# Optimization experiments

Measured on AMD Instinct MI355X. Metric: run time of the kernel, lower is better.

The kernel has to match this reference:

```python
import jax, jax.numpy as jnp
import numpy as np
from jax import lax

U = 512      # rnn_units
A = 512      # attn_units
E = 300      # embed_dim
VS = 30000   # source vocab
VT = 30000   # target vocab
S = 64       # source len
T = 32       # target len
B = 32       # batch


def gru_step(h, x, Wih, Whh, bih, bhh):
    # PyTorch GRU cell: r,z,n gate order
    gi = x @ Wih.T + bih
    gh = h @ Whh.T + bhh
    ir, iz, i_n = jnp.split(gi, 3, axis=-1)
    hr, hz, h_n = jnp.split(gh, 3, axis=-1)
    r = jax.nn.sigmoid(ir + hr)
    z = jax.nn.sigmoid(iz + hz)
    n = jnp.tanh(i_n + r * h_n)
    return (1.0 - z) * n + z * h


def setup_inputs() -> dict:
    key = jax.random.key(0)
    ks = jax.random.split(key, 24)
    w = lambda k, shape, s=0.08: jax.random.normal(k, shape, dtype=jnp.float32) * s
    inp = {
        "emb_src": w(ks[0], (VS, E), 0.1),
        "emb_trg": w(ks[1], (VT, E), 0.1),
        # encoder bidirectional GRU (fwd/bwd directions)
        "enc_Wih_f": w(ks[2], (3 * U, E)), "enc_Whh_f": w(ks[3], (3 * U, U)),
        "enc_bih_f": w(ks[4], (3 * U,)), "enc_bhh_f": w(ks[5], (3 * U,)),
        "enc_Wih_b": w(ks[6], (3 * U, E)), "enc_Whh_b": w(ks[7], (3 * U, U)),
        "enc_bih_b": w(ks[8], (3 * U,)), "enc_bhh_b": w(ks[9], (3 * U,)),
        "enc_Wfc": w(ks[10], (U, 2 * U)), "enc_bfc": w(ks[11], (U,)),
        # attention fc: attn_in = 3U -> A
        "attn_W": w(ks[12], (A, 3 * U)), "attn_b": w(ks[13], (A,)),
        # decoder GRU: input = 2U + E
        "dec_Wih": w(ks[14], (3 * U, 2 * U + E)), "dec_Whh": w(ks[15], (3 * U, U)),
        "dec_bih": w(ks[16], (3 * U,)), "dec_bhh": w(ks[17], (3 * U,)),
        # decoder output fc: 3U + E -> VT
        "dec_Wfc": w(ks[18], (VT, 3 * U + E)), "dec_bfc": w(ks[19], (VT,)),
        "source": jax.random.randint(ks[20], (S, B), 0, VS, dtype=jnp.int32),
        "target": jax.random.randint(ks[21], (T, B), 0, VT, dtype=jnp.int32),
    }
    return inp


def reference(emb_src, emb_trg,
              enc_Wih_f, enc_Whh_f, enc_bih_f, enc_bhh_f,
              enc_Wih_b, enc_Whh_b, enc_bih_b, enc_bhh_b,
              enc_Wfc, enc_bfc, attn_W, attn_b,
              dec_Wih, dec_Whh, dec_bih, dec_bhh, dec_Wfc, dec_bfc,
              source, target):
    # dropout in eval mode (identity); teacher_forcing fixed to 1.0 (deterministic)
    batch = source.shape[1]
    emb = emb_src[source]  # [S, B, E]
    h0 = jnp.zeros((batch, U), dtype=emb.dtype)

    def fstep(h, x):
        h2 = gru_step(h, x, enc_Wih_f, enc_Whh_f, enc_bih_f, enc_bhh_f)
        return h2, h2

    def bstep(h, x):
        h2 = gru_step(h, x, enc_Wih_b, enc_Whh_b, enc_bih_b, enc_bhh_b)
        return h2, h2

    hf, outs_f = lax.scan(fstep, h0, emb)
    hb, outs_b = lax.scan(bstep, h0, emb[::-1])
    outs_b = outs_b[::-1]
    enc_outputs = jnp.concatenate([outs_f, outs_b], axis=-1)        # [S, B, 2U]
    state = jnp.tanh(jnp.concatenate([hf, hb], axis=-1) @ enc_Wfc.T + enc_bfc)  # [B, U]
    enc_bt = jnp.transpose(enc_outputs, (1, 0, 2))                  # [B, S, 2U]

    def dstep(st, tok):
        emb_t = emb_trg[tok]                                        # [B, E]
        dec_rep = jnp.broadcast_to(st[:, None, :], (batch, enc_bt.shape[1], U))
        comb = jnp.concatenate([dec_rep, enc_bt], axis=2)           # [B, S, 3U]
        scores = jnp.tanh(jnp.einsum('bsf,af->bsa', comb, attn_W) + attn_b).sum(-1)
        wts = jax.nn.softmax(scores, axis=1)                        # [B, S]
        ctx = jnp.einsum('bs,bsh->bh', wts, enc_bt)                 # [B, 2U]
        x = jnp.concatenate([emb_t, ctx], axis=1)                   # [B, E+2U]
        st2 = gru_step(st, x, dec_Wih, dec_Whh, dec_bih, dec_bhh)   # [B, U]
        logits = jnp.concatenate([st2, ctx, emb_t], axis=1) @ dec_Wfc.T + dec_bfc
        return st2, logits

    _, logits = lax.scan(dstep, state, target[:-1])                 # [T-1, B, VT]
    zero_row = jnp.zeros((1, batch, dec_Wfc.shape[0]), dtype=logits.dtype)
    return jnp.concatenate([zero_row, logits], axis=0)              # [T, B, VT]
```

## Files before the change

### kernel.cpp

```cpp
#include <hip/hip_runtime.h>

#define UU 512
#define EE 300
#define VTT 30000
#define SS 64
#define TT 32
#define BB 32

typedef unsigned short u16;
typedef short s8v __attribute__((ext_vector_type(8)));
typedef unsigned short us4 __attribute__((ext_vector_type(4)));
typedef float f4v __attribute__((ext_vector_type(4)));

__device__ __forceinline__ float bf2f(u16 v){
  union { unsigned u; float f; } x; x.u = ((unsigned)v) << 16; return x.f;
}
__device__ __forceinline__ u16 f2bf(float f){
  union { float f; unsigned u; } x; x.f = f;
  unsigned r = x.u + 0x7FFFu + ((x.u >> 16) & 1u);
  return (u16)(r >> 16);
}
__device__ __forceinline__ float sigm(float x){ return 1.f / (1.f + __expf(-x)); }
__device__ __forceinline__ float ftanh(float x){
  float t = __expf(-2.f * fabsf(x));
  float r = (1.f - t) / (1.f + t);
  return x < 0.f ? -r : r;
}
__device__ __forceinline__ int imin(int a, int b){ return a < b ? a : b; }

__device__ __forceinline__ void gll16(const u16* g, u16* l){
  __builtin_amdgcn_global_load_lds(
      (const __attribute__((address_space(1))) void*)g,
      (__attribute__((address_space(3))) void*)l, 16, 0, 0);
}

__global__ void k_init(float* __restrict__ hF, float* __restrict__ out,
                       u16* __restrict__ Xl, float* __restrict__ hbfF){
  int i = blockIdx.x * 256 + threadIdx.x;
  if(i < 4*BB*UU) hF[i] = 0.f;
  if(i < BB*VTT) out[i] = 0.f;
  if(i < 992*20){
    int r = i / 20, c = i - r*20;
    Xl[(size_t)r*1856 + 1836 + c] = 0;
  }
  if(i < 65536) hbfF[i] = 0.f;
}

__global__ void k_embsrc(const float* __restrict__ emb, const int* __restrict__ src,
                         u16* __restrict__ X){
  int i = blockIdx.x * 256 + threadIdx.x;
  if(i >= SS*BB*320) return;
  int tb = i / 320, k = i - tb*320;
  X[i] = (k < EE) ? f2bf(emb[(size_t)src[tb]*EE + k]) : (u16)0;
}

__global__ void k_embT(const float* __restrict__ emb, const int* __restrict__ tgt,
                       u16* __restrict__ X, u16* __restrict__ Xl){
  int i = blockIdx.x * 256 + threadIdx.x;
  if(i >= 992*320) return;
  int r = i / 320, k = i - r*320;
  u16 v = (k < EE) ? f2bf(emb[(size_t)tgt[r]*EE + k]) : (u16)0;
  X[i] = v;
  if(k < EE) Xl[(size_t)r*1856 + 1536 + k] = v;
}

__global__ void k_cvt(const float* __restrict__ src, int srs, int cofs, int take,
                      u16* __restrict__ dst, int cdst){
  int r = blockIdx.x;
  const float* s = src + (size_t)r*srs + cofs;
  u16* d = dst + (size_t)r*cdst;
  for(int c4 = threadIdx.x; c4 < (cdst >> 2); c4 += blockDim.x){
    us4 o;
    if(c4*4 < take){
      f4v v = *(const f4v*)(s + c4*4);
      o[0]=f2bf(v[0]); o[1]=f2bf(v[1]); o[2]=f2bf(v[2]); o[3]=f2bf(v[3]);
    } else o = (us4){0,0,0,0};
    *(us4*)(d + c4*4) = o;
  }
}

__global__ void k_wprep(const float* __restrict__ W, int ldw, int colofs,
                        int gstr, int ng, int ubstr, int NKF, int passes,
                        int total, u16* __restrict__ out){
  int flat = blockIdx.x * 256 + threadIdx.x;
  if(flat >= total) return;
  int l = flat & 63;
  int g = (flat >> 6) % ng;
  int kf = (flat / (64*ng)) % NKF;
  int ub = flat / (64*ng*NKF);
  int row = g*gstr + ub*ubstr + (l & 15);
  int col = colofs + kf*32 + ((l >> 4) << 3);
  const float* s = W + (size_t)row*ldw + col;
  f4v v0 = *(const f4v*)(s);
  f4v v1 = *(const f4v*)(s + 4);
  size_t base = ((((size_t)(ub*NKF + kf)*ng + g)*passes)*64 + l)*8;
  us4 h0, h1;
  h0[0]=f2bf(v0[0]); h0[1]=f2bf(v0[1]); h0[2]=f2bf(v0[2]); h0[3]=f2bf(v0[3]);
  h1[0]=f2bf(v1[0]); h1[1]=f2bf(v1[1]); h1[2]=f2bf(v1[2]); h1[3]=f2bf(v1[3]);
// ... 42 lines not shown
  for(int k0 = 0; k0 < K; k0 += 32){
    __syncthreads();
    gll16(Ag0 + k0, Al0); gll16(Ag1 + k0, Al1);
    gll16(Bg0 + k0, Bl0); gll16(Bg1 + k0, Bl1);
    __syncthreads();
    s8v af[4], bfv[4];
    #pragma unroll
    for(int mi = 0; mi < 4; mi++)
      af[mi] = *(const s8v*)(Asl + (wm*64 + mi*16 + lm)*32 + lq*8);
    #pragma unroll
    for(int nj = 0; nj < 4; nj++)
      bfv[nj] = *(const s8v*)(Bsl + (wn*64 + nj*16 + lm)*32 + lq*8);
    #pragma unroll
    for(int mi = 0; mi < 4; mi++)
      #pragma unroll
      for(int nj = 0; nj < 4; nj++)
        acc[mi][nj] = __builtin_amdgcn_mfma_f32_16x16x32_bf16(af[mi], bfv[nj], acc[mi][nj], 0, 0, 0);
  }
  #pragma unroll
  for(int nj = 0; nj < 4; nj++){
    int n = n0 + wn*64 + nj*16 + lm;
    if(n < N){
      float bv = bias[n];
      #pragma unroll
      for(int mi = 0; mi < 4; mi++){
        #pragma unroll
        for(int rg = 0; rg < 4; rg++){
          int m = m0 + wm*64 + mi*16 + lq*4 + rg;
          if(m < M) C[(size_t)(m + mofs)*ldc + n] = acc[mi][nj][rg] + bv;
        }
      }
    }
  }
}

__global__ __launch_bounds__(256) void k_gemm_bf(
    const u16* __restrict__ A, int lda, const u16* __restrict__ B, int ldb,
    const float* __restrict__ bias, float* __restrict__ C, int ldc, int mofs,
    int M, int N, int K){
  gemm_body(blockIdx.x*128, blockIdx.y*128, A, lda, B, ldb, bias, C, ldc, mofs, M, N, K);
}

__global__ __launch_bounds__(256) void k_gemm_lg(
    const u16* __restrict__ A, int lda, const u16* __restrict__ B, int ldb,
    const float* __restrict__ bias, float* __restrict__ C, int ldc, int mofs,
    int M, int N, int K){
  int id = blockIdx.x;
  int x = id & 7, j = id >> 3;
  int m = j & 7, p = (j & ~7) | x;
  if(p * 128 >= N) return;
  gemm_body(m*128, p*128, A, lda, B, ldb, bias, C, ldc, mofs, M, N, K);
}

__global__ __launch_bounds__(64) void k_encs(int t,
    const float* __restrict__ gi_f, const float* __restrict__ gi_b,
    const u16* __restrict__ Wenc,
    const float* __restrict__ bhh_f, const float* __restrict__ bhh_b,
    float* __restrict__ hF, u16* __restrict__ hbf, u16* __restrict__ enc){
  int dir = blockIdx.x >> 5;
  int ub  = blockIdx.x & 31;
  int l = threadIdx.x;
  int par = t & 1;
  int te = dir ? (SS-1-t) : t;
  const float* gi  = (dir ? gi_b : gi_f) + (size_t)(te*BB)*1536;
  const float* bhh = dir ? bhh_b : bhh_f;
  const u16* Wslab = Wenc + ((size_t)(dir*32 + ub))*49152;
  const u16* Asrc  = hbf + (size_t)(par*2 + dir)*32768;
  u16* Adst        = hbf + (size_t)((par^1)*2 + dir)*32768;
  const float* hin = hF + (size_t)(dir*2 + par)*(BB*UU);
  float* hout      = hF + (size_t)(dir*2 + (par^1))*(BB*UU);
  __shared__ __align__(16) u16 Ab[16384];
  __shared__ __align__(16) u16 Bb[24576];
  f4v acc[2][3];
  #pragma unroll
  for(int i = 0; i < 2; i++)
    #pragma unroll
    for(int j = 0; j < 3; j++) acc[i][j] = (f4v){0.f,0.f,0.f,0.f};
  for(int c = 0; c < 2; c++){
    __syncthreads();
    #pragma unroll
    for(int i = 0; i < 32; i++) gll16(Asrc + c*16384 + i*512 + l*8, Ab + i*512);
    #pragma unroll
    for(int i = 0; i < 48; i++) gll16(Wslab + c*24576 + i*512 + l*8, Bb + i*512);
    __syncthreads();
    #pragma unroll
    for(int kf = 0; kf < 8; kf++){
      s8v a[2][2], bw[3][2];
      #pragma unroll
      for(int mf = 0; mf < 2; mf++)
        #pragma unroll
        for(int p = 0; p < 2; p++)
          a[mf][p] = *(const s8v*)(Ab + ((kf*2+mf)*2+p)*512 + l*8);
      #pragma unroll
      for(int g = 0; g < 3; g++)
        #pragma unroll
        for(int p = 0; p < 2; p++)
          bw[g][p] = *(const s8v*)(Bb + ((kf*3+g)*2+p)*512 + l*8);
      #pragma unroll
      for(int mf = 0; mf < 2; mf++)
        #pragma unroll
        for(int g = 0; g < 3; g++){
          acc[mf][g] = __builtin_amdgcn_mfma_f32_16x16x32_bf16(a[mf][0], bw[g][0], acc[mf][g], 0, 0, 0);
          acc[mf][g] = __builtin_amdgcn_mfma_f32_16x16x32_bf16(a[mf][1], bw[g][0], acc[mf][g], 0, 0, 0);
          acc[mf][g] = __builtin_amdgcn_mfma_f32_16x16x32_bf16(a[mf][0], bw[g][1], acc[mf][g], 0, 0, 0);
        }
    }
  }
  float* ghs = (float*)Ab;
  int lm = l & 15, lq = l >> 4;
  #pragma unroll
  for(int mf = 0; mf < 2; mf++)
    #pragma unroll
    for(int g = 0; g < 3; g++)
      #pragma unroll
      for(int rg = 0; rg < 4; rg++)
        ghs[(g*16 + lm)*32 + mf*16 + lq*4 + rg] = acc[mf][g][rg];
  __syncthreads();
  #pragma unroll
  for(int it = 0; it < 8; it++){
    int idx = it*64 + l;
    int b = idx & 31, ulu = idx >> 5;
    int u = ub*16 + ulu;
    float ghr = ghs[(ulu)*32 + b]      + bhh[u];
    float ghz = ghs[(16 + ulu)*32 + b] + bhh[512 + u];
    float ghn = ghs[(32 + ulu)*32 + b] + bhh[1024 + u];
    const float* gb = gi + b*1536 + u;
    float r = sigm(gb[0] + ghr);
    float z = sigm(gb[512] + ghz);
    float n = ftanh(gb[1024] + r*ghn);
    float hold = hin[b*512 + u];
    float h2 = (1.f - z)*n + z*hold;
    hout[b*512 + u] = h2;
    enc[(size_t)(b*SS + te)*1024 + dir*512 + u] = f2bf(h2);
    u16 hi = f2bf(h2);
    float lo = h2 - bf2f(hi);
    int kf = u >> 5, mf = b >> 4, l2 = ((u >> 3) & 3)*16 + (b & 15), e = u & 7;
    int base = ((kf*2 + mf)*2)*512 + l2*8 + e;
    Adst[base]       = hi;
    Adst[base + 512] = f2bf(lo);
  }
}

__global__ __launch_bounds__(256) void k_encfc(
    const float* __restrict__ h, const float* __restrict__ Wfc,
    const float* __restrict__ bfc, float* __restrict__ st, u16* __restrict__ Ast0){
  int b = blockIdx.x;
  __shared__ __align__(16) float hc[1024];
  for(int i = threadIdx.x; i < 512; i += 256){
    hc[i]       = h[0*BB*UU + b*UU + i];
    hc[512 + i] = h[2*BB*UU + b*UU + i];
  }
  __syncthreads();
  for(int u = threadIdx.x; u < 512; u += 256){
    const float* w = Wfc + u*1024;
    float a = 0.f;
    for(int k = 0; k < 1024; k += 4){
      f4v x = *(const f4v*)(hc + k);
      f4v wv = *(const f4v*)(w + k);
      a += x[0]*wv[0] + x[1]*wv[1] + x[2]*wv[2] + x[3]*wv[3];
    }
    float sv = ftanh(a + bfc[u]);
    st[b*UU + u] = sv;
    u16 hi = f2bf(sv);
    float lo = sv - bf2f(hi);
    int kf = u >> 5, mf = b >> 4, l2 = ((u >> 3) & 3)*16 + (b & 15), e = u & 7;
    int base = ((kf*2 + mf)*2)*512 + l2*8 + e;
    Ast0[base]       = hi;
    Ast0[base + 512] = f2bf(lo);
  }
}

__global__ __launch_bounds__(64) void k_dq(
    const u16* __restrict__ Ast_in, const u16* __restrict__ Wqp,
    float* __restrict__ qG){
  int ub = blockIdx.x;
  int l = threadIdx.x;
  const u16* Ws = Wqp + (size_t)ub*32768;
  __shared__ __align__(16) u16 Ab[16384];
  __shared__ __align__(16) u16 Bb[16384];
  f4v acc[2][2];
  #pragma unroll
  for(int i = 0; i < 2; i++)
    #pragma unroll
    for(int j = 0; j < 2; j++) acc[i][j] = (f4v){0.f,0.f,0.f,0.f};
  for(int c = 0; c < 2; c++){
    __syncthreads();
    #pragma unroll
    for(int i = 0; i < 32; i++) gll16(Ast_in + c*16384 + i*512 + l*8, Ab + i*512);
    #pragma unroll
    for(int i = 0; i < 32; i++) gll16(Ws + c*16384 + i*512 + l*8, Bb + i*512);
    __syncthreads();
    #pragma unroll
    for(int kf = 0; kf < 8; kf++){
      s8v a[2][2], bw[2][2];
      #pragma unroll
      for(int mf = 0; mf < 2; mf++)
        #pragma unroll
        for(int p = 0; p < 2; p++){
          a[mf][p]  = *(const s8v*)(Ab + ((kf*2+mf)*2+p)*512 + l*8);
          bw[mf][p] = *(const s8v*)(Bb + ((kf*2+mf)*2+p)*512 + l*8);
        }
      #pragma unroll
      for(int mf = 0; mf < 2; mf++)
        #pragma unroll
        for(int g = 0; g < 2; g++){
          acc[mf][g] = __builtin_amdgcn_mfma_f32_16x16x32_bf16(a[mf][0], bw[g][0], acc[mf][g], 0, 0, 0);
          acc[mf][g] = __builtin_amdgcn_mfma_f32_16x16x32_bf16(a[mf][1], bw[g][0], acc[mf][g], 0, 0, 0);
          acc[mf][g] = __builtin_amdgcn_mfma_f32_16x16x32_bf16(a[mf][0], bw[g][1], acc[mf][g], 0, 0, 0);
        }
    }
  }
  int lm = l & 15, lq = l >> 4;
  #pragma unroll
  for(int mf = 0; mf < 2; mf++)
    #pragma unroll
    for(int g = 0; g < 2; g++)
      #pragma unroll
      for(int rg = 0; rg < 4; rg++){
        int a_ = ub*32 + g*16 + lm;
        int b  = mf*16 + lq*4 + rg;
        qG[b*512 + (a_ & 31)*16 + (a_ >> 5)] = acc[mf][g][rg];
      }
}

__global__ __launch_bounds__(1024) void k_dattn(int t,
    const float* __restrict__ qG, const float* __restrict__ P,
    const u16* __restrict__ enc, u16* __restrict__ Actx, u16* __restrict__ Xl){
  int b = blockIdx.x, tid = threadIdx.x;
  __shared__ float qvt[512];
  __shared__ float wv[64];
  if(tid < 512) qvt[tid] = qG[b*512 + tid];
  __syncthreads();
  {
    int s = tid >> 4, part = tid & 15;
    const float* Pb = P + (size_t)(b*SS + s)*512 + part*32;
    float ps = 0.f;
    #pragma unroll
    for(int i = 0; i < 32; i += 4){
      f4v pv = *(const f4v*)(Pb + i);
      ps += ftanh(pv[0] + qvt[(i+0)*16 + part]);
      ps += ftanh(pv[1] + qvt[(i+1)*16 + part]);
      ps += ftanh(pv[2] + qvt[(i+2)*16 + part]);
      ps += ftanh(pv[3] + qvt[(i+3)*16 + part]);
    }
    #pragma unroll
    for(int o = 1; o < 16; o <<= 1) ps += __shfl_xor(ps, o);
    if(part == 0) wv[s] = ps;
  }
  __syncthreads();
  if(tid < 64){
    float sc = wv[tid];
    float m = sc;
    for(int o = 32; o > 0; o >>= 1) m = fmaxf(m, __shfl_xor(m, o));
    float e = __expf(sc - m);
    float ssum = e;
    for(int o = 32; o > 0; o >>= 1) ssum += __shfl_xor(ssum, o);
    wv[tid] = e / ssum;
  }
  __syncthreads();
  int rowX = t*BB + b;
  int j = tid;
  float acc = 0.f;
  const u16* eb = enc + (size_t)(b*SS)*1024 + j;
  #pragma unroll 8
  for(int s2 = 0; s2 < SS; s2++)
    acc += wv[s2] * bf2f(eb[(size_t)s2*1024]);
  u16 cb = f2bf(acc);
  Xl[(size_t)rowX*1856 + 512 + j] = cb;
  int kf = j >> 5, mf = b >> 4, l2 = ((j >> 3) & 3)*16 + (b & 15), e = j & 7;
  Actx[(size_t)(kf*2 + mf)*512 + l2*8 + e] = cb;
}

__global__ __launch_bounds__(64) void k_dgru(int t,
    const float* __restrict__ st_in, float* __restrict__ st_out,
    const u16* __restrict__ Actx, const u16* __restrict__ Ast_in,
    u16* __restrict__ Ast_out,
    const u16* __restrict__ Wdc, const u16* __restrict__ Wds,
    const float* __restrict__ giE, const float* __restrict__ bhh,
    u16* __restrict__ Xl){
  int ub = blockIdx.x;
  int l = threadIdx.x;
  const u16* Wdcs = Wdc + (size_t)ub*49152;
  const u16* Wdss = Wds + (size_t)ub*49152;
  __shared__ __align__(16) u16 Ab[16384];
  __shared__ __align__(16) u16 Bb[24576];
  f4v accI[2][3], accH[2][3];
  #pragma unroll
  for(int i = 0; i < 2; i++)
    #pragma unroll
    for(int j = 0; j < 3; j++){
      accI[i][j] = (f4v){0.f,0.f,0.f,0.f};
      accH[i][j] = (f4v){0.f,0.f,0.f,0.f};
    }
  for(int c = 0; c < 2; c++){
    __syncthreads();
    #pragma unroll
    for(int i = 0; i < 32; i++) gll16(Actx + c*16384 + i*512 + l*8, Ab + i*512);
    #pragma unroll
    for(int i = 0; i < 48; i++) gll16(Wdcs + c*24576 + i*512 + l*8, Bb + i*512);
    __syncthreads();
    #pragma unroll
    for(int kf = 0; kf < 16; kf++){
      s8v a[2], bw[3];
      #pragma unroll
      for(int mf = 0; mf < 2; mf++)
        a[mf] = *(const s8v*)(Ab + (kf*2+mf)*512 + l*8);
      #pragma unroll
      for(int g = 0; g < 3; g++)
        bw[g] = *(const s8v*)(Bb + (kf*3+g)*512 + l*8);
      #pragma unroll
      for(int mf = 0; mf < 2; mf++)
        #pragma unroll
        for(int g = 0; g < 3; g++)
          accI[mf][g] = __builtin_amdgcn_mfma_f32_16x16x32_bf16(a[mf], bw[g], accI[mf][g], 0, 0, 0);
    }
  }
  for(int c = 0; c < 2; c++){
    __syncthreads();
    #pragma unroll
    for(int i = 0; i < 32; i++) gll16(Ast_in + c*16384 + i*512 + l*8, Ab + i*512);
    #pragma unroll
    for(int i = 0; i < 48; i++) gll16(Wdss + c*24576 + i*512 + l*8, Bb + i*512);
    __syncthreads();
    #pragma unroll
    for(int kf = 0; kf < 8; kf++){
      s8v a[2][2], bw[3][2];
      #pragma unroll
      for(int mf = 0; mf < 2; mf++)
        #pragma unroll
        for(int p = 0; p < 2; p++)
          a[mf][p] = *(const s8v*)(Ab + ((kf*2+mf)*2+p)*512 + l*8);
      #pragma unroll
      for(int g = 0; g < 3; g++)
        #pragma unroll
        for(int p = 0; p < 2; p++)
          bw[g][p] = *(const s8v*)(Bb + ((kf*3+g)*2+p)*512 + l*8);
      #pragma unroll
      for(int mf = 0; mf < 2; mf++)
        #pragma unroll
        for(int g = 0; g < 3; g++){
          accH[mf][g] = __builtin_amdgcn_mfma_f32_16x16x32_bf16(a[mf][0], bw[g][0], accH[mf][g], 0, 0, 0);
          accH[mf][g] = __builtin_amdgcn_mfma_f32_16x16x32_bf16(a[mf][1], bw[g][0], accH[mf][g], 0, 0, 0);
          accH[mf][g] = __builtin_amdgcn_mfma_f32_16x16x32_bf16(a[mf][0], bw[g][1], accH[mf][g], 0, 0, 0);
        }
    }
  }
  float* ghsI = (float*)Ab;
  float* ghsH = ghsI + 1536;
  int lm = l & 15, lq = l >> 4;
  #pragma unroll
  for(int mf = 0; mf < 2; mf++)
    #pragma unroll
    for(int g = 0; g < 3; g++)
      #pragma unroll
      for(int rg = 0; rg < 4; rg++){
        int o = (g*16 + lm)*32 + mf*16 + lq*4 + rg;
        ghsI[o] = accI[mf][g][rg];
        ghsH[o] = accH[mf][g][rg];
      }
  __syncthreads();
  #pragma unroll
  for(int it = 0; it < 8; it++){
    int idx = it*64 + l;
    int b = idx & 31, ulu = idx >> 5;
    int u = ub*16 + ulu;
    int xrow = t*BB + b;
    const float* ge = giE + (size_t)xrow*1536 + u;
    float gIr = ghsI[(ulu)*32 + b]      + ge[0];
    float gIz = ghsI[(16 + ulu)*32 + b] + ge[512];
    float gIn = ghsI[(32 + ulu)*32 + b] + ge[1024];
    float gHr = ghsH[(ulu)*32 + b]      + bhh[u];
    float gHz = ghsH[(16 + ulu)*32 + b] + bhh[512 + u];
    float gHn = ghsH[(32 + ulu)*32 + b] + bhh[1024 + u];
    float r = sigm(gIr + gHr);
    float z = sigm(gIz + gHz);
    float n = ftanh(gIn + r*gHn);
    float hold = st_in[b*512 + u];
    float h2 = (1.f - z)*n + z*hold;
    st_out[b*512 + u] = h2;
    Xl[(size_t)xrow*1856 + u] = f2bf(h2);
    u16 hi = f2bf(h2);
    float lo = h2 - bf2f(hi);
    int kf = u >> 5, mf = b >> 4, l2 = ((u >> 3) & 3)*16 + (b & 15), e = u & 7;
    int base = ((kf*2 + mf)*2)*512 + l2*8 + e;
    Ast_out[base]       = hi;
    Ast_out[base + 512] = f2bf(lo);
  }
}

extern "C" void kernel_launch(void* const* d_in, const int* in_sizes, int n_in,
                              void* d_out, int out_size, void* d_ws, size_t ws_size,
                              hipStream_t stream){
  (void)in_sizes; (void)n_in; (void)out_size; (void)ws_size;
  const float* emb_src = (const float*)d_in[0];
  const float* emb_trg = (const float*)d_in[1];
  const float* eWih_f  = (const float*)d_in[2];
  const float* eWhh_f  = (const float*)d_in[3];
  const float* ebih_f  = (const float*)d_in[4];
  const float* ebhh_f  = (const float*)d_in[5];
  const float* eWih_b  = (const float*)d_in[6];
  const float* eWhh_b  = (const float*)d_in[7];
  const float* ebih_b  = (const float*)d_in[8];
  const float* ebhh_b  = (const float*)d_in[9];
  const float* Wfc     = (const float*)d_in[10];
  const float* bfc     = (const float*)d_in[11];
  const float* attn_W  = (const float*)d_in[12];
  const float* attn_b  = (const float*)d_in[13];
  const float* dWih    = (const float*)d_in[14];
  const float* dWhh    = (const float*)d_in[15];
  const float* dbih    = (const float*)d_in[16];
  const float* dbhh    = (const float*)d_in[17];
  const float* dWfc    = (const float*)d_in[18];
  const float* dbfc    = (const float*)d_in[19];
  const int* source    = (const int*)d_in[20];
  const int* target    = (const int*)d_in[21];
  float* out = (float*)d_out;
  float* wsf = (float*)d_ws;

  float* P    = wsf;
  float* hF   = P + (size_t)2048*512;
  float* st   = hF + 65536;
  float* qG   = st + 32768;
  float* giE  = qG + 16384;
  u16* enc   = (u16*)(giE + (size_t)992*1536);
  u16* Xl    = enc + (size_t)2048*1024;
  u16* Xsrc  = Xl + (size_t)992*1856;
  u16* WihF  = Xsrc + (size_t)2048*320;
  u16* WihB  = WihF + (size_t)1536*320;
  u16* WihE  = WihB + (size_t)1536*320;
  u16* AttnW = WihE + (size_t)1536*320;
  u16* Wenc  = AttnW + (size_t)512*1024;
  u16* Wdc   = Wenc + (size_t)2*32*49152;
  u16* Wds   = Wdc + (size_t)32*49152;
  u16* Wqp   = Wds + (size_t)32*49152;
  u16* hbf   = Wqp + (size_t)16*32768;
  u16* Actx  = hbf + (size_t)4*32768;
  u16* Ast   = Actx + 32768;
  u16* endu  = Ast + (size_t)2*32768;
  float* gi_f = (float*)endu;
  float* gi_b = gi_f + (size_t)2048*1536;
  u16* WfcB  = endu;
  u16* EmbT  = Xsrc;

  k_init<<<3750, 256, 0, stream>>>(hF, out, Xl, (float*)hbf);
  k_embsrc<<<2560, 256, 0, stream>>>(emb_src, source, Xsrc);
  k_cvt<<<1536, 256, 0, stream>>>(eWih_f, 300, 0, 300, WihF, 320);
  k_cvt<<<1536, 256, 0, stream>>>(eWih_b, 300, 0, 300, WihB, 320);
  k_cvt<<<1536, 256, 0, stream>>>(dWih, 1324, 0, 300, WihE, 320);
  k_cvt<<<512, 256, 0, stream>>>(attn_W, 1536, 512, 1024, AttnW, 1024);
  k_wprep<<<384, 256, 0, stream>>>(eWhh_f, 512, 0, 512, 3, 16, 16, 2, 98304, Wenc);
  k_wprep<<<384, 256, 0, stream>>>(eWhh_b, 512, 0, 512, 3, 16, 16, 2, 98304, Wenc + (size_t)32*49152);
  k_wprep<<<768, 256, 0, stream>>>(dWih, 1324, 300, 512, 3, 16, 32, 1, 196608, Wdc);
  k_wprep<<<384, 256, 0, stream>>>(dWhh, 512, 0, 512, 3, 16, 16, 2, 98304, Wds);
  k_wprep<<<128, 256, 0, stream>>>(attn_W, 1536, 0, 16, 2, 32, 16, 2, 32768, Wqp);
  k_gemm_bf<<<dim3(16,12), 256, 0, stream>>>(Xsrc, 320, WihF, 320, ebih_f, gi_f, 1536, 0, 2048, 1536, 320);
  k_gemm_bf<<<dim3(16,12), 256, 0, stream>>>(Xsrc, 320, WihB, 320, ebih_b, gi_b, 1536, 0, 2048, 1536, 320);
  for(int t = 0; t < SS; t++)
    k_encs<<<64, 64, 0, stream>>>(t, gi_f, gi_b, Wenc, ebhh_f, ebhh_b, hF, hbf, enc);
  k_encfc<<<BB, 256, 0, stream>>>(hF, Wfc, bfc, st, Ast);
  k_gemm_bf<<<dim3(16,4), 256, 0, stream>>>(enc, 1024, AttnW, 1024, attn_b, P, 512, 0, 2048, 512, 1024);
  k_embT<<<1240, 256, 0, stream>>>(emb_trg, target, EmbT, Xl);
  k_gemm_bf<<<dim3(8,12), 256, 0, stream>>>(EmbT, 320, WihE, 320, dbih, giE, 1536, 0, 992, 1536, 320);
  for(int t = 0; t < TT-1; t++){
    int par = t & 1;
    k_dq<<<16, 64, 0, stream>>>(Ast + par*32768, Wqp, qG);
    k_dattn<<<BB, 1024, 0, stream>>>(t, qG, P, enc, Actx, Xl);
    k_dgru<<<32, 64, 0, stream>>>(t, st + par*16384, st + (par^1)*16384,
                                  Actx, Ast + par*32768, Ast + (par^1)*32768,
                                  Wdc, Wds, giE, dbhh, Xl);
  }
  k_cvt<<<30000, 256, 0, stream>>>(dWfc, 1836, 0, 1836, WfcB, 1856);
  k_gemm_lg<<<1920, 256, 0, stream>>>(Xl, 1856, WfcB, 1856, dbfc, out, VTT, 32, 992, VTT, 1856);
}
```

Before: 2.205 ms.

## Make encoder and decoder recurrences persistent kernels with grid barriers

```diff
diff --git a/kernel.cpp b/kernel.cpp
--- a/kernel.cpp
+++ b/kernel.cpp
@@ -34,8 +34,27 @@
       (__attribute__((address_space(3))) void*)l, 16, 0, 0);
 }
 
+__device__ __forceinline__ void gbar(unsigned* cnt, unsigned* gen,
+                                     unsigned nblk, unsigned target){
+  __syncthreads();
+  if(threadIdx.x == 0){
+    __threadfence();
+    if(atomicAdd(cnt, 1u) == nblk - 1u){
+      __hip_atomic_store(cnt, 0u, __ATOMIC_RELAXED, __HIP_MEMORY_SCOPE_AGENT);
+      __threadfence();
+      __hip_atomic_store(gen, target, __ATOMIC_RELEASE, __HIP_MEMORY_SCOPE_AGENT);
+    } else {
+      while(__hip_atomic_load(gen, __ATOMIC_ACQUIRE, __HIP_MEMORY_SCOPE_AGENT) < target)
+        __builtin_amdgcn_s_sleep(2);
+    }
+    __threadfence();
+  }
+  __syncthreads();
+}
+
 __global__ void k_init(float* __restrict__ hF, float* __restrict__ out,
-                       u16* __restrict__ Xl, float* __restrict__ hbfF){
+                       u16* __restrict__ Xl, float* __restrict__ hbfF,
+                       unsigned* __restrict__ bars){
   int i = blockIdx.x * 256 + threadIdx.x;
   if(i < 4*BB*UU) hF[i] = 0.f;
   if(i < BB*VTT) out[i] = 0.f;
@@ -44,6 +63,7 @@
     Xl[(size_t)r*1856 + 1836 + c] = 0;
   }
   if(i < 65536) hbfF[i] = 0.f;
+  if(i < 128) bars[i] = 0u;
 }
 
 __global__ void k_embsrc(const float* __restrict__ emb, const int* __restrict__ src,
@@ -192,92 +212,100 @@
   gemm_body(m*128, p*128, A, lda, B, ldb, bias, C, ldc, mofs, M, N, K);
 }
 
-__global__ __launch_bounds__(64) void k_encs(int t,
+__global__ __launch_bounds__(64) void k_encp(
     const float* __restrict__ gi_f, const float* __restrict__ gi_b,
     const u16* __restrict__ Wenc,
     const float* __restrict__ bhh_f, const float* __restrict__ bhh_b,
-    float* __restrict__ hF, u16* __restrict__ hbf, u16* __restrict__ enc){
+    float* __restrict__ hF, u16* __restrict__ hbf, u16* __restrict__ enc,
+    unsigned* __restrict__ bars){
   int dir = blockIdx.x >> 5;
   int ub  = blockIdx.x & 31;
   int l = threadIdx.x;
-  int par = t & 1;
-  int te = dir ? (SS-1-t) : t;
-  const float* gi  = (dir ? gi_b : gi_f) + (size_t)(te*BB)*1536;
+  const float* giB = dir ? gi_b : gi_f;
   const float* bhh = dir ? bhh_b : bhh_f;
   const u16* Wslab = Wenc + ((size_t)(dir*32 + ub))*49152;
-  const u16* Asrc  = hbf + (size_t)(par*2 + dir)*32768;
-  u16* Adst        = hbf + (size_t)((par^1)*2 + dir)*32768;
-  const float* hin = hF + (size_t)(dir*2 + par)*(BB*UU);
-  float* hout      = hF + (size_t)(dir*2 + (par^1))*(BB*UU);
+  unsigned* cnt = bars + dir*32;
+  unsigned* gen = bars + dir*32 + 16;
+  __shared__ __align__(16) u16 WL[49152];
   __shared__ __align__(16) u16 Ab[16384];
-  __shared__ __align__(16) u16 Bb[24576];
-  f4v acc[2][3];
-  #pragma unroll
-  for(int i = 0; i < 2; i++)
+  #pragma unroll 1
+  for(int i = 0; i < 96; i++) gll16(Wslab + i*512 + l*8, WL + i*512);
+  int lm = l & 15, lq = l >> 4;
+  for(int t = 0; t < SS; t++){
+    int par = t & 1;
+    int te = dir ? (SS-1-t) : t;
+    const float* gi = giB + (size_t)(te*BB)*1536;
+    const u16* Asrc = hbf + (size_t)(par*2 + dir)*32768;
+    u16* Adst       = hbf + (size_t)((par^1)*2 + dir)*32768;
+    const float* hin = hF + (size_t)(dir*2 + par)*(BB*UU);
+    float* hout      = hF + (size_t)(dir*2 + (par^1))*(BB*UU);
+    f4v acc[2][3];
     #pragma unroll
-    for(int j = 0; j < 3; j++) acc[i][j] = (f4v){0.f,0.f,0.f,0.f};
-  for(int c = 0; c < 2; c++){
+    for(int i = 0; i < 2; i++)
+      #pragma unroll
+      for(int j = 0; j < 3; j++) acc[i][j] = (f4v){0.f,0.f,0.f,0.f};
+    for(int c = 0; c < 2; c++){
+      __syncthreads();
+      #pragma unroll 1
+      for(int i = 0; i < 32; i++) gll16(Asrc + c*16384 + i*512 + l*8, Ab + i*512);
+      __syncthreads();
+      #pragma unroll
+      for(int kf = 0; kf < 8; kf++){
+        s8v a[2][2], bw[3][2];
+        #pragma unroll
+        for(int mf = 0; mf < 2; mf++)
+          #pragma unroll
+          for(int p = 0; p < 2; p++)
+            a[mf][p] = *(const s8v*)(Ab + ((kf*2+mf)*2+p)*512 + l*8);
+        #pragma unroll
+        for(int g = 0; g < 3; g++)
+          #pragma unroll
+          for(int p = 0; p < 2; p++)
+            bw[g][p] = *(const s8v*)(WL + c*24576 + ((kf*3+g)*2+p)*512 + l*8);
+        #pragma unroll
+        for(int mf = 0; mf < 2; mf++)
+          #pragma unroll
+          for(int g = 0; g < 3; g++){
+            acc[mf][g] = __builtin_amdgcn_mfma_f32_16x16x32_bf16(a[mf][0], bw[g][0], acc[mf][g], 0, 0, 0);
+            acc[mf][g] = __builtin_amdgcn_mfma_f32_16x16x32_bf16(a[mf][1], bw[g][0], acc[mf][g], 0, 0, 0);
+            acc[mf][g] = __builtin_amdgcn_mfma_f32_16x16x32_bf16(a[mf][0], bw[g][1], acc[mf][g], 0, 0, 0);
+          }
+      }
+    }
+    __syncthreads();
+    float* ghs = (float*)Ab;
+    #pragma unroll
+    for(int mf = 0; mf < 2; mf++)
+      #pragma unroll
+      for(int g = 0; g < 3; g++)
+        #pragma unroll
+        for(int rg = 0; rg < 4; rg++)
+          ghs[(g*16 + lm)*32 + mf*16 + lq*4 + rg] = acc[mf][g][rg];
     __syncthreads();
     #pragma unroll
-    for(int i = 0; i < 32; i++) gll16(Asrc + c*16384 + i*512 + l*8, Ab + i*512);
-    #pragma unroll
-    for(int i = 0; i < 48; i++) gll16(Wslab + c*24576 + i*512 + l*8, Bb + i*512);
-    __syncthreads();
-    #pragma unroll
-    for(int kf = 0; kf < 8; kf++){
-      s8v a[2][2], bw[3][2];
-      #pragma unroll
-      for(int mf = 0; mf < 2; mf++)
-        #pragma unroll
-        for(int p = 0; p < 2; p++)
-          a[mf][p] = *(const s8v*)(Ab + ((kf*2+mf)*2+p)*512 + l*8);
-      #pragma unroll
-      for(int g = 0; g < 3; g++)
-        #pragma unroll
-        for(int p = 0; p < 2; p++)
-          bw[g][p] = *(const s8v*)(Bb + ((kf*3+g)*2+p)*512 + l*8);
-      #pragma unroll
-      for(int mf = 0; mf < 2; mf++)
-        #pragma unroll
-        for(int g = 0; g < 3; g++){
-          acc[mf][g] = __builtin_amdgcn_mfma_f32_16x16x32_bf16(a[mf][0], bw[g][0], acc[mf][g], 0, 0, 0);
-          acc[mf][g] = __builtin_amdgcn_mfma_f32_16x16x32_bf16(a[mf][1], bw[g][0], acc[mf][g], 0, 0, 0);
-          acc[mf][g] = __builtin_amdgcn_mfma_f32_16x16x32_bf16(a[mf][0], bw[g][1], acc[mf][g], 0, 0, 0);
-        }
-    }
-  }
-  float* ghs = (float*)Ab;
-  int lm = l & 15, lq = l >> 4;
-  #pragma unroll
-  for(int mf = 0; mf < 2; mf++)
-    #pragma unroll
-    for(int g = 0; g < 3; g++)
-      #pragma unroll
-      for(int rg = 0; rg < 4; rg++)
-        ghs[(g*16 + lm)*32 + mf*16 + lq*4 + rg] = acc[mf][g][rg];
-  __syncthreads();
-  #pragma unroll
-  for(int it = 0; it < 8; it++){
-    int idx = it*64 + l;
-    int b = idx & 31, ulu = idx >> 5;
-    int u = ub*16 + ulu;
-    float ghr = ghs[(ulu)*32 + b]      + bhh[u];
-    float ghz = ghs[(16 + ulu)*32 + b] + bhh[512 + u];
-    float ghn = ghs[(32 + ulu)*32 + b] + bhh[1024 + u];
-    const float* gb = gi + b*1536 + u;
-    float r = sigm(gb[0] + ghr);
-    float z = sigm(gb[512] + ghz);
-    float n = ftanh(gb[1024] + r*ghn);
-    float hold = hin[b*512 + u];
-    float h2 = (1.f - z)*n + z*hold;
-    hout[b*512 + u] = h2;
-    enc[(size_t)(b*SS + te)*1024 + dir*512 + u] = f2bf(h2);
-    u16 hi = f2bf(h2);
-    float lo = h2 - bf2f(hi);
-    int kf = u >> 5, mf = b >> 4, l2 = ((u >> 3) & 3)*16 + (b & 15), e = u & 7;
-    int base = ((kf*2 + mf)*2)*512 + l2*8 + e;
-    Adst[base]       = hi;
-    Adst[base + 512] = f2bf(lo);
+    for(int it = 0; it < 8; it++){
+      int idx = it*64 + l;
+      int b = idx & 31, ulu = idx >> 5;
+      int u = ub*16 + ulu;
+      float ghr = ghs[(ulu)*32 + b]      + bhh[u];
+      float ghz = ghs[(16 + ulu)*32 + b] + bhh[512 + u];
+      float ghn = ghs[(32 + ulu)*32 + b] + bhh[1024 + u];
+      const float* gb = gi + b*1536 + u;
+      float r = sigm(gb[0] + ghr);
+      float z = sigm(gb[512] + ghz);
+      float n = ftanh(gb[1024] + r*ghn);
+      float hold = hin[b*512 + u];
+      float h2 = (1.f - z)*n + z*hold;
+      hout[b*512 + u] = h2;
+      enc[(size_t)(b*SS + te)*1024 + dir*512 + u] = f2bf(h2);
+      u16 hi = f2bf(h2);
+      float lo = h2 - bf2f(hi);
+      int kf = u >> 5, mf = b >> 4, l2 = ((u >> 3) & 3)*16 + (b & 15), e = u & 7;
+      int base = ((kf*2 + mf)*2)*512 + l2*8 + e;
+      Adst[base]       = hi;
+      Adst[base + 512] = f2bf(lo);
+    }
+    if(t < SS-1) gbar(cnt, gen, 32u, (unsigned)(t+1));
   }
 }
 
@@ -310,221 +338,244 @@
   }
 }
 
-__global__ __launch_bounds__(64) void k_dq(
-    const u16* __restrict__ Ast_in, const u16* __restrict__ Wqp,
-    float* __restrict__ qG){
-  int ub = blockIdx.x;
-  int l = threadIdx.x;
-  const u16* Ws = Wqp + (size_t)ub*32768;
+__global__ __launch_bounds__(256) void k_decp(
+    float* __restrict__ st, const float* __restrict__ P,
+    const u16* __restrict__ enc, const u16* __restrict__ Wqp,
+    const u16* __restrict__ Wdc, const u16* __restrict__ Wds,
+    u16* __restrict__ Actx, u16* __restrict__ Ast,
+    float* __restrict__ qGp,
+    const float* __restrict__ giE, const float* __restrict__ bhh,
+    u16* __restrict__ Xl, unsigned* __restrict__ bars){
+  int bid = blockIdx.x;
+  int tid = threadIdx.x;
+  int l = tid & 63, w = tid >> 6;
+  int lm = l & 15, lq = l >> 4;
+  unsigned* cnt = bars + 64;
+  unsigned* gen = bars + 96;
   __shared__ __align__(16) u16 Ab[16384];
-  __shared__ __align__(16) u16 Bb[16384];
-  f4v acc[2][2];
-  #pragma unroll
-  for(int i = 0; i < 2; i++)
-    #pragma unroll
-    for(int j = 0; j < 2; j++) acc[i][j] = (f4v){0.f,0.f,0.f,0.f};
-  for(int c = 0; c < 2; c++){
-    __syncthreads();
-    #pragma unroll
-    for(int i = 0; i < 32; i++) gll16(Ast_in + c*16384 + i*512 + l*8, Ab + i*512);
-    #pragma unroll
-    for(int i = 0; i < 32; i++) gll16(Ws + c*16384 + i*512 + l*8, Bb + i*512);
-    __syncthreads();
-    #pragma unroll
-    for(int kf = 0; kf < 8; kf++){
-      s8v a[2][2], bw[2][2];
-      #pragma unroll
-      for(int mf = 0; mf < 2; mf++)
-        #pragma unroll
-        for(int p = 0; p < 2; p++){
-          a[mf][p]  = *(const s8v*)(Ab + ((kf*2+mf)*2+p)*512 + l*8);
-          bw[mf][p] = *(const s8v*)(Bb + ((kf*2+mf)*2+p)*512 + l*8);
-        }
-      #pragma unroll
-      for(int mf = 0; mf < 2; mf++)
-        #pragma unroll
-        for(int g = 0; g < 2; g++){
-          acc[mf][g] = __builtin_amdgcn_mfma_f32_16x16x32_bf16(a[mf][0], bw[g][0], acc[mf][g], 0, 0, 0);
-          acc[mf][g] = __builtin_amdgcn_mfma_f32_16x16x32_bf16(a[mf][1], bw[g][0], acc[mf][g], 0, 0, 0);
-          acc[mf][g] = __builtin_amdgcn_mfma_f32_16x16x32_bf16(a[mf][0], bw[g][1], acc[mf][g], 0, 0, 0);
-        }
-    }
-  }
-  int lm = l & 15, lq = l >> 4;
-  #pragma unroll
-  for(int mf = 0; mf < 2; mf++)
-    #pragma unroll
-    for(int g = 0; g < 2; g++)
-      #pragma unroll
-      for(int rg = 0; rg < 4; rg++){
-        int a_ = ub*32 + g*16 + lm;
-        int b  = mf*16 + lq*4 + rg;
-        qG[b*512 + (a_ & 31)*16 + (a_ >> 5)] = acc[mf][g][rg];
-      }
-}
-
-__global__ __launch_bounds__(1024) void k_dattn(int t,
-    const float* __restrict__ qG, const float* __restrict__ P,
-    const u16* __restrict__ enc, u16* __restrict__ Actx, u16* __restrict__ Xl){
-  int b = blockIdx.x, tid = threadIdx.x;
+  __shared__ __align__(16) u16 Bb[24576];
   __shared__ float qvt[512];
   __shared__ float wv[64];
-  if(tid < 512) qvt[tid] = qG[b*512 + tid];
-  __syncthreads();
-  {
-    int s = tid >> 4, part = tid & 15;
-    const float* Pb = P + (size_t)(b*SS + s)*512 + part*32;
-    float ps = 0.f;
-    #pragma unroll
-    for(int i = 0; i < 32; i += 4){
-      f4v pv = *(const f4v*)(Pb + i);
-      ps += ftanh(pv[0] + qvt[(i+0)*16 + part]);
-      ps += ftanh(pv[1] + qvt[(i+1)*16 + part]);
-      ps += ftanh(pv[2] + qvt[(i+2)*16 + part]);
-      ps += ftanh(pv[3] + qvt[(i+3)*16 + part]);
-    }
-    #pragma unroll
-    for(int o = 1; o < 16; o <<= 1) ps += __shfl_xor(ps, o);
-    if(part == 0) wv[s] = ps;
-  }
-  __syncthreads();
-  if(tid < 64){
-    float sc = wv[tid];
-    float m = sc;
-    for(int o = 32; o > 0; o >>= 1) m = fmaxf(m, __shfl_xor(m, o));
-    float e = __expf(sc - m);
-    float ssum = e;
-    for(int o = 32; o > 0; o >>= 1) ssum += __shfl_xor(ssum, o);
-    wv[tid] = e / ssum;
-  }
-  __syncthreads();
-  int rowX = t*BB + b;
-  int j = tid;
-  float acc = 0.f;
-  const u16* eb = enc + (size_t)(b*SS)*1024 + j;
-  #pragma unroll 8
-  for(int s2 = 0; s2 < SS; s2++)
-    acc += wv[s2] * bf2f(eb[(size_t)s2*1024]);
-  u16 cb = f2bf(acc);
-  Xl[(size_t)rowX*1856 + 512 + j] = cb;
-  int kf = j >> 5, mf = b >> 4, l2 = ((j >> 3) & 3)*16 + (b & 15), e = j & 7;
-  Actx[(size_t)(kf*2 + mf)*512 + l2*8 + e] = cb;
-}
-
-__global__ __launch_bounds__(64) void k_dgru(int t,
-    const float* __restrict__ st_in, float* __restrict__ st_out,
-    const u16* __restrict__ Actx, const u16* __restrict__ Ast_in,
-    u16* __restrict__ Ast_out,
-    const u16* __restrict__ Wdc, const u16* __restrict__ Wds,
-    const float* __restrict__ giE, const float* __restrict__ bhh,
-    u16* __restrict__ Xl){
-  int ub = blockIdx.x;
-  int l = threadIdx.x;
-  const u16* Wdcs = Wdc + (size_t)ub*49152;
-  const u16* Wdss = Wds + (size_t)ub*49152;
-  __shared__ __align__(16) u16 Ab[16384];
-  __shared__ __align__(16) u16 Bb[24576];
-  f4v accI[2][3], accH[2][3];
-  #pragma unroll
-  for(int i = 0; i < 2; i++)
-    #pragma unroll
-    for(int j = 0; j < 3; j++){
-      accI[i][j] = (f4v){0.f,0.f,0.f,0.f};
-      accH[i][j] = (f4v){0.f,0.f,0.f,0.f};
-    }
-  for(int c = 0; c < 2; c++){
+  unsigned tgt = 0;
+  int ubq = bid >> 1, cq = bid & 1;
+  const u16* Wq  = Wqp + (size_t)ubq*32768 + cq*16384;
+  const u16* Wdcs = Wdc + (size_t)bid*49152;
+  const u16* Wdss = Wds + (size_t)bid*49152;
+  for(int t = 0; t < TT-1; t++){
+    int par = t & 1;
+    const u16* AstI = Ast + par*32768;
+    u16* AstO       = Ast + (par^1)*32768;
+    const float* stin = st + par*16384;
+    float* stout      = st + (par^1)*16384;
+    if(w == 0){
+      #pragma unroll 1
+      for(int i = 0; i < 32; i++) gll16(AstI + cq*16384 + i*512 + l*8, Ab + i*512);
+      #pragma unroll 1
+      for(int i = 0; i < 32; i++) gll16(Wq + i*512 + l*8, Bb + i*512);
+    }
     __syncthreads();
-    #pragma unroll
-    for(int i = 0; i < 32; i++) gll16(Actx + c*16384 + i*512 + l*8, Ab + i*512);
-    #pragma unroll
-    for(int i = 0; i < 48; i++) gll16(Wdcs + c*24576 + i*512 + l*8, Bb + i*512);
-    __syncthreads();
-    #pragma unroll
-    for(int kf = 0; kf < 16; kf++){
-      s8v a[2], bw[3];
+    if(w == 0){
+      f4v qa[2][2];
+      #pragma unroll
+      for(int i = 0; i < 2; i++)
+        #pragma unroll
+        for(int j = 0; j < 2; j++) qa[i][j] = (f4v){0.f,0.f,0.f,0.f};
+      #pragma unroll
+      for(int kf = 0; kf < 8; kf++){
+        s8v a[2][2], bw[2][2];
+        #pragma unroll
+        for(int mf = 0; mf < 2; mf++)
+          #pragma unroll
+          for(int p = 0; p < 2; p++){
+            a[mf][p]  = *(const s8v*)(Ab + ((kf*2+mf)*2+p)*512 + l*8);
+            bw[mf][p] = *(const s8v*)(Bb + ((kf*2+mf)*2+p)*512 + l*8);
+          }
+        #pragma unroll
+        for(int mf = 0; mf < 2; mf++)
+          #pragma unroll
+          for(int g = 0; g < 2; g++){
+            qa[mf][g] = __builtin_amdgcn_mfma_f32_16x16x32_bf16(a[mf][0], bw[g][0], qa[mf][g], 0, 0, 0);
+            qa[mf][g] = __builtin_amdgcn_mfma_f32_16x16x32_bf16(a[mf][1], bw[g][0], qa[mf][g], 0, 0, 0);
+            qa[mf][g] = __builtin_amdgcn_mfma_f32_16x16x32_bf16(a[mf][0], bw[g][1], qa[mf][g], 0, 0, 0);
+          }
+      }
+      float* qout = qGp + cq*16384;
       #pragma unroll
       for(int mf = 0; mf < 2; mf++)
-        a[mf] = *(const s8v*)(Ab + (kf*2+mf)*512 + l*8);
-      #pragma unroll
-      for(int g = 0; g < 3; g++)
-        bw[g] = *(const s8v*)(Bb + (kf*3+g)*512 + l*8);
+        #pragma unroll
+        for(int g = 0; g < 2; g++)
+          #pragma unroll
+          for(int rg = 0; rg < 4; rg++){
+            int a_ = ubq*32 + g*16 + lm;
+            int b_ = mf*16 + lq*4 + rg;
+            qout[b_*512 + (a_ & 31)*16 + (a_ >> 5)] = qa[mf][g][rg];
+          }
+    }
+    gbar(cnt, gen, 32u, ++tgt);
+    {
+      int b = bid;
+      for(int i = tid; i < 512; i += 256)
+        qvt[i] = qGp[b*512 + i] + qGp[16384 + b*512 + i];
+      __syncthreads();
+      {
+        int s = tid >> 2, part = tid & 3;
+        const float* Pb = P + (size_t)(b*SS + s)*512 + part*128;
+        float ps = 0.f;
+        #pragma unroll 8
+        for(int i = 0; i < 128; i += 4){
+          f4v pv = *(const f4v*)(Pb + i);
+          int a0 = part*128 + i;
+          ps += ftanh(pv[0] + qvt[((a0+0)&31)*16 + ((a0+0)>>5)]);
+          ps += ftanh(pv[1] + qvt[((a0+1)&31)*16 + ((a0+1)>>5)]);
+          ps += ftanh(pv[2] + qvt[((a0+2)&31)*16 + ((a0+2)>>5)]);
+          ps += ftanh(pv[3] + qvt[((a0+3)&31)*16 + ((a0+3)>>5)]);
+        }
+        ps += __shfl_xor(ps, 1);
+        ps += __shfl_xor(ps, 2);
+        if(part == 0) wv[s] = ps;
+      }
+      __syncthreads();
+      if(tid < 64){
+        float sc = wv[tid];
+        float m = sc;
+        for(int o = 32; o > 0; o >>= 1) m = fmaxf(m, __shfl_xor(m, o));
+        float e = __expf(sc - m);
+        float ssum = e;
+        for(int o = 32; o > 0; o >>= 1) ssum += __shfl_xor(ssum, o);
+        wv[tid] = e / ssum;
+      }
+      __syncthreads();
+      int rowX = t*BB + b;
+      #pragma unroll
+      for(int jj = 0; jj < 4; jj++){
+        int j = jj*256 + tid;
+        float acc2 = 0.f;
+        const u16* eb = enc + (size_t)(b*SS)*1024 + j;
+        #pragma unroll 8
+        for(int s2 = 0; s2 < SS; s2++)
+          acc2 += wv[s2] * bf2f(eb[(size_t)s2*1024]);
+        u16 cb = f2bf(acc2);
+        Xl[(size_t)rowX*1856 + 512 + j] = cb;
+        int kf = j >> 5, mf = b >> 4, l2 = ((j >> 3) & 3)*16 + (b & 15), e = j & 7;
+        Actx[(size_t)(kf*2 + mf)*512 + l2*8 + e] = cb;
+      }
+    }
+    gbar(cnt, gen, 32u, ++tgt);
+    {
+      int ub = bid;
+      f4v accI[2][3], accH[2][3];
+      #pragma unroll
+      for(int i = 0; i < 2; i++)
+        #pragma unroll
+        for(int j = 0; j < 3; j++){
+          accI[i][j] = (f4v){0.f,0.f,0.f,0.f};
+          accH[i][j] = (f4v){0.f,0.f,0.f,0.f};
+        }
+      #pragma unroll 1
+      for(int sp = 0; sp < 4; sp++){
+        const u16* Asub = (sp < 2) ? (Actx + sp*16384) : (AstI + (sp-2)*16384);
+        const u16* Bsub = (sp < 2) ? (Wdcs + sp*24576) : (Wdss + (sp-2)*24576);
+        __syncthreads();
+        #pragma unroll 1
+        for(int i = 0; i < 20; i++){
+          int r = w*20 + i;
+          const u16* src = (r < 32) ? (Asub + r*512) : (Bsub + (size_t)(r-32)*512);
+          u16* dst = (r < 32) ? (Ab + r*512) : (Bb + (r-32)*512);
+          gll16(src + l*8, dst);
+        }
+        __syncthreads();
+        if(sp < 2){
+          #pragma unroll
+          for(int kk = 0; kk < 4; kk++){
+            int kf = w*4 + kk;
+            s8v a0 = *(const s8v*)(Ab + (kf*2+0)*512 + l*8);
+            s8v a1 = *(const s8v*)(Ab + (kf*2+1)*512 + l*8);
+            s8v b0 = *(const s8v*)(Bb + (kf*3+0)*512 + l*8);
+            s8v b1 = *(const s8v*)(Bb + (kf*3+1)*512 + l*8);
+            s8v b2 = *(const s8v*)(Bb + (kf*3+2)*512 + l*8);
+            accI[0][0] = __builtin_amdgcn_mfma_f32_16x16x32_bf16(a0, b0, accI[0][0], 0, 0, 0);
+            accI[0][1] = __builtin_amdgcn_mfma_f32_16x16x32_bf16(a0, b1, accI[0][1], 0, 0, 0);
+            accI[0][2] = __builtin_amdgcn_mfma_f32_16x16x32_bf16(a0, b2, accI[0][2], 0, 0, 0);
+            accI[1][0] = __builtin_amdgcn_mfma_f32_16x16x32_bf16(a1, b0, accI[1][0], 0, 0, 0);
+            accI[1][1] = __builtin_amdgcn_mfma_f32_16x16x32_bf16(a1, b1, accI[1][1], 0, 0, 0);
+            accI[1][2] = __builtin_amdgcn_mfma_f32_16x16x32_bf16(a1, b2, accI[1][2], 0, 0, 0);
+          }
+        } else {
+          #pragma unroll
+          for(int kk = 0; kk < 2; kk++){
+            int kf = w*2 + kk;
+            s8v a[2][2], bw[3][2];
+            #pragma unroll
+            for(int mf = 0; mf < 2; mf++)
+              #pragma unroll
+              for(int p = 0; p < 2; p++)
+                a[mf][p] = *(const s8v*)(Ab + ((kf*2+mf)*2+p)*512 + l*8);
+            #pragma unroll
+            for(int g = 0; g < 3; g++)
+              #pragma unroll
+              for(int p = 0; p < 2; p++)
+                bw[g][p] = *(const s8v*)(Bb + ((kf*3+g)*2+p)*512 + l*8);
+            #pragma unroll
+            for(int mf = 0; mf < 2; mf++)
+              #pragma unroll
+              for(int g = 0; g < 3; g++){
+                accH[mf][g] = __builtin_amdgcn_mfma_f32_16x16x32_bf16(a[mf][0], bw[g][0], accH[mf][g], 0, 0, 0);
+                accH[mf][g] = __builtin_amdgcn_mfma_f32_16x16x32_bf16(a[mf][1], bw[g][0], accH[mf][g], 0, 0, 0);
+                accH[mf][g] = __builtin_amdgcn_mfma_f32_16x16x32_bf16(a[mf][0], bw[g][1], accH[mf][g], 0, 0, 0);
+              }
+          }
+        }
+      }
+      __syncthreads();
+      float* ghsI = (float*)Bb;
+      float* ghsH = (float*)Ab;
       #pragma unroll
       for(int mf = 0; mf < 2; mf++)
         #pragma unroll
         for(int g = 0; g < 3; g++)
-          accI[mf][g] = __builtin_amdgcn_mfma_f32_16x16x32_bf16(a[mf], bw[g], accI[mf][g], 0, 0, 0);
-    }
-  }
-  for(int c = 0; c < 2; c++){
-    __syncthreads();
-    #pragma unroll
-    for(int i = 0; i < 32; i++) gll16(Ast_in + c*16384 + i*512 + l*8, Ab + i*512);
-    #pragma unroll
-    for(int i = 0; i < 48; i++) gll16(Wdss + c*24576 + i*512 + l*8, Bb + i*512);
-    __syncthreads();
-    #pragma unroll
-    for(int kf = 0; kf < 8; kf++){
-      s8v a[2][2], bw[3][2];
-      #pragma unroll
-      for(int mf = 0; mf < 2; mf++)
-        #pragma unroll
-        for(int p = 0; p < 2; p++)
-          a[mf][p] = *(const s8v*)(Ab + ((kf*2+mf)*2+p)*512 + l*8);
-      #pragma unroll
-      for(int g = 0; g < 3; g++)
-        #pragma unroll
-        for(int p = 0; p < 2; p++)
-          bw[g][p] = *(const s8v*)(Bb + ((kf*3+g)*2+p)*512 + l*8);
-      #pragma unroll
-      for(int mf = 0; mf < 2; mf++)
-        #pragma unroll
-        for(int g = 0; g < 3; g++){
-          accH[mf][g] = __builtin_amdgcn_mfma_f32_16x16x32_bf16(a[mf][0], bw[g][0], accH[mf][g], 0, 0, 0);
-          accH[mf][g] = __builtin_amdgcn_mfma_f32_16x16x32_bf16(a[mf][1], bw[g][0], accH[mf][g], 0, 0, 0);
-          accH[mf][g] = __builtin_amdgcn_mfma_f32_16x16x32_bf16(a[mf][0], bw[g][1], accH[mf][g], 0, 0, 0);
+          #pragma unroll
+          for(int rg = 0; rg < 4; rg++){
+            int o = w*1536 + (g*16 + lm)*32 + mf*16 + lq*4 + rg;
+            ghsI[o] = accI[mf][g][rg];
+            ghsH[o] = accH[mf][g][rg];
+          }
+      __syncthreads();
+      #pragma unroll
+      for(int it = 0; it < 2; it++){
+        int idx = it*256 + tid;
+        int b2 = idx & 31, ulu = idx >> 5;
+        int u = ub*16 + ulu;
+        int xrow = t*BB + b2;
+        float gIr=0.f, gIz=0.f, gIn=0.f, gHr=0.f, gHz=0.f, gHn=0.f;
+        #pragma unroll
+        for(int ww = 0; ww < 4; ww++){
+          int o = ww*1536;
+          gIr += ghsI[o + (ulu)*32 + b2];
+          gIz += ghsI[o + (16 + ulu)*32 + b2];
+          gIn += ghsI[o + (32 + ulu)*32 + b2];
+          gHr += ghsH[o + (ulu)*32 + b2];
+          gHz += ghsH[o + (16 + ulu)*32 + b2];
+          gHn += ghsH[o + (32 + ulu)*32 + b2];
         }
-    }
-  }
-  float* ghsI = (float*)Ab;
-  float* ghsH = ghsI + 1536;
-  int lm = l & 15, lq = l >> 4;
-  #pragma unroll
-  for(int mf = 0; mf < 2; mf++)
-    #pragma unroll
-    for(int g = 0; g < 3; g++)
-      #pragma unroll
-      for(int rg = 0; rg < 4; rg++){
-        int o = (g*16 + lm)*32 + mf*16 + lq*4 + rg;
-        ghsI[o] = accI[mf][g][rg];
-        ghsH[o] = accH[mf][g][rg];
-      }
-  __syncthreads();
-  #pragma unroll
-  for(int it = 0; it < 8; it++){
-    int idx = it*64 + l;
-    int b = idx & 31, ulu = idx >> 5;
-    int u = ub*16 + ulu;
-    int xrow = t*BB + b;
-    const float* ge = giE + (size_t)xrow*1536 + u;
-    float gIr = ghsI[(ulu)*32 + b]      + ge[0];
-    float gIz = ghsI[(16 + ulu)*32 + b] + ge[512];
-    float gIn = ghsI[(32 + ulu)*32 + b] + ge[1024];
-    float gHr = ghsH[(ulu)*32 + b]      + bhh[u];
-    float gHz = ghsH[(16 + ulu)*32 + b] + bhh[512 + u];
-    float gHn = ghsH[(32 + ulu)*32 + b] + bhh[1024 + u];
-    float r = sigm(gIr + gHr);
-    float z = sigm(gIz + gHz);
-    float n = ftanh(gIn + r*gHn);
-    float hold = st_in[b*512 + u];
-    float h2 = (1.f - z)*n + z*hold;
-    st_out[b*512 + u] = h2;
-    Xl[(size_t)xrow*1856 + u] = f2bf(h2);
-    u16 hi = f2bf(h2);
-    float lo = h2 - bf2f(hi);
-    int kf = u >> 5, mf = b >> 4, l2 = ((u >> 3) & 3)*16 + (b & 15), e = u & 7;
-    int base = ((kf*2 + mf)*2)*512 + l2*8 + e;
-    Ast_out[base]       = hi;
-    Ast_out[base + 512] = f2bf(lo);
+        const float* ge = giE + (size_t)xrow*1536 + u;
+        gIr += ge[0]; gIz += ge[512]; gIn += ge[1024];
+        gHr += bhh[u]; gHz += bhh[512 + u]; gHn += bhh[1024 + u];
+        float r = sigm(gIr + gHr);
+        float z = sigm(gIz + gHz);
+        float n = ftanh(gIn + r*gHn);
+        float hold = stin[b2*512 + u];
+        float h2 = (1.f - z)*n + z*hold;
+        stout[b2*512 + u] = h2;
+        Xl[(size_t)xrow*1856 + u] = f2bf(h2);
+        u16 hi = f2bf(h2);
+        float lo = h2 - bf2f(hi);
+        int kf2 = u >> 5, mf2 = b2 >> 4, l2 = ((u >> 3) & 3)*16 + (b2 & 15), e = u & 7;
+        int base = ((kf2*2 + mf2)*2)*512 + l2*8 + e;
+        AstO[base]       = hi;
+        AstO[base + 512] = f2bf(lo);
+      }
+    }
+    if(t < TT-2) gbar(cnt, gen, 32u, ++tgt);
   }
 }
 
@@ -560,8 +611,8 @@
   float* P    = wsf;
   float* hF   = P + (size_t)2048*512;
   float* st   = hF + 65536;
-  float* qG   = st + 32768;
-  float* giE  = qG + 16384;
+  float* qGp  = st + 32768;
+  float* giE  = qGp + 32768;
   u16* enc   = (u16*)(giE + (size_t)992*1536);
   u16* Xl    = enc + (size_t)2048*1024;
   u16* Xsrc  = Xl + (size_t)992*1856;
@@ -576,13 +627,14 @@
   u16* hbf   = Wqp + (size_t)16*32768;
   u16* Actx  = hbf + (size_t)4*32768;
   u16* Ast   = Actx + 32768;
-  u16* endu  = Ast + (size_t)2*32768;
+  unsigned* bars = (unsigned*)(Ast + (size_t)2*32768);
+  u16* endu  = (u16*)(bars + 128);
   float* gi_f = (float*)endu;
   float* gi_b = gi_f + (size_t)2048*1536;
   u16* WfcB  = endu;
   u16* EmbT  = Xsrc;
 
-  k_init<<<3750, 256, 0, stream>>>(hF, out, Xl, (float*)hbf);
+  k_init<<<3750, 256, 0, stream>>>(hF, out, Xl, (float*)hbf, bars);
   k_embsrc<<<2560, 256, 0, stream>>>(emb_src, source, Xsrc);
   k_cvt<<<1536, 256, 0, stream>>>(eWih_f, 300, 0, 300, WihF, 320);
   k_cvt<<<1536, 256, 0, stream>>>(eWih_b, 300, 0, 300, WihB, 320);
@@ -595,20 +647,13 @@
   k_wprep<<<128, 256, 0, stream>>>(attn_W, 1536, 0, 16, 2, 32, 16, 2, 32768, Wqp);
   k_gemm_bf<<<dim3(16,12), 256, 0, stream>>>(Xsrc, 320, WihF, 320, ebih_f, gi_f, 1536, 0, 2048, 1536, 320);
   k_gemm_bf<<<dim3(16,12), 256, 0, stream>>>(Xsrc, 320, WihB, 320, ebih_b, gi_b, 1536, 0, 2048, 1536, 320);
-  for(int t = 0; t < SS; t++)
-    k_encs<<<64, 64, 0, stream>>>(t, gi_f, gi_b, Wenc, ebhh_f, ebhh_b, hF, hbf, enc);
+  k_encp<<<64, 64, 0, stream>>>(gi_f, gi_b, Wenc, ebhh_f, ebhh_b, hF, hbf, enc, bars);
   k_encfc<<<BB, 256, 0, stream>>>(hF, Wfc, bfc, st, Ast);
   k_gemm_bf<<<dim3(16,4), 256, 0, stream>>>(enc, 1024, AttnW, 1024, attn_b, P, 512, 0, 2048, 512, 1024);
   k_embT<<<1240, 256, 0, stream>>>(emb_trg, target, EmbT, Xl);
   k_gemm_bf<<<dim3(8,12), 256, 0, stream>>>(EmbT, 320, WihE, 320, dbih, giE, 1536, 0, 992, 1536, 320);
-  for(int t = 0; t < TT-1; t++){
-    int par = t & 1;
-    k_dq<<<16, 64, 0, stream>>>(Ast + par*32768, Wqp, qG);
-    k_dattn<<<BB, 1024, 0, stream>>>(t, qG, P, enc, Actx, Xl);
-    k_dgru<<<32, 64, 0, stream>>>(t, st + par*16384, st + (par^1)*16384,
-                                  Actx, Ast + par*32768, Ast + (par^1)*32768,
-                                  Wdc, Wds, giE, dbhh, Xl);
-  }
+  k_decp<<<32, 256, 0, stream>>>(st, P, enc, Wqp, Wdc, Wds, Actx, Ast, qGp,
+                                 giE, dbhh, Xl, bars);
   k_cvt<<<30000, 256, 0, stream>>>(dWfc, 1836, 0, 1836, WfcB, 1856);
   k_gemm_lg<<<1920, 256, 0, stream>>>(Xl, 1856, WfcB, 1856, dbfc, out, VTT, 32, 992, VTT, 1856);
 }
```

New measurement: 2.841 ms. 1.29x slower.
